# Performance work log

Hardware: AMD Instinct MI355X
Metric: run time of the kernel (lower is better)

Reference implementation:

```python
import jax, jax.numpy as jnp
import numpy as np

NUM_CLASSES = 80
NUM_TOP_QUERIES = 300
MASK_THRESHOLD = 0.5
OUT_SIZE = 480  # fixed original image size (all orig_target_sizes == 480)


def setup_inputs() -> dict:
    key = jax.random.key(0)
    k1, k2, k3 = jax.random.split(key, 3)
    B, Q, C, Hm, Wm = 2, 300, NUM_CLASSES, 128, 128
    pred_logits = jax.random.normal(k1, (B, Q, C), dtype=jnp.float32)
    pred_boxes = jax.random.uniform(k2, (B, Q, 4), dtype=jnp.float32)  # cxcywh in [0,1]
    pred_masks = jax.random.normal(k3, (B, Q, Hm, Wm), dtype=jnp.float32)
    orig_target_sizes = jnp.ones((B, 2), dtype=jnp.float32) * OUT_SIZE
    return {
        'pred_logits': pred_logits,
        'pred_boxes': pred_boxes,
        'pred_masks': pred_masks,
        'orig_target_sizes': orig_target_sizes,
    }


def _box_cxcywh_to_xyxy(boxes):
    cx, cy, w, h = jnp.split(boxes, 4, axis=-1)
    return jnp.concatenate([cx - 0.5 * w, cy - 0.5 * h, cx + 0.5 * w, cy + 0.5 * h], axis=-1)


def reference(pred_logits, pred_boxes, pred_masks, orig_target_sizes):
    B, Q, C = pred_logits.shape
    Hm, Wm = pred_masks.shape[-2:]
    K = NUM_TOP_QUERIES

    # box conversion + scaling to original image size ([s0,s1,s0,s1] like repeat(1,2))
    scale = jnp.tile(orig_target_sizes, (1, 2))[:, None, :]  # [B,1,4]
    scaled_boxes = _box_cxcywh_to_xyxy(pred_boxes) * scale    # [B,Q,4]

    # focal-loss path: sigmoid scores, flattened top-k over (Q*C)
    scores = jax.nn.sigmoid(pred_logits).reshape(B, Q * C)
    top_scores, top_indices = jax.lax.top_k(scores, K)        # [B,K]
    top_labels = top_indices % C
    query_indices = top_indices // C                          # [B,K]

    selected_boxes = jnp.take_along_axis(scaled_boxes, query_indices[..., None], axis=1)  # [B,K,4]

    # per-sample mask selection + sigmoid + bilinear upsample (align_corners=False)
    sel_masks = jnp.take_along_axis(pred_masks, query_indices[..., None, None], axis=1)   # [B,K,Hm,Wm]
    mask_probs = jax.nn.sigmoid(sel_masks)
    up = jax.vmap(lambda m: jax.image.resize(m, (OUT_SIZE, OUT_SIZE), 'bilinear'))(
        mask_probs.reshape(B * K, Hm, Wm)
    ).reshape(B, K, OUT_SIZE, OUT_SIZE)
    binary_masks = up > MASK_THRESHOLD                        # [B,K,H,W] bool (torch adds channel dim of 1)

    return top_scores, top_labels, selected_boxes, binary_masks
```

## Files before the change

kernel.cpp:

```cpp
#include <hip/hip_runtime.h>
#include <math.h>

#define BATCH 2
#define NQ    300
#define NC    80
#define NFLAT (NQ * NC)
#define TOPK  300
#define HM    128
#define OUTS  480
#define NBKT  4096
#define CAP   4096

#define INVSCALEF 0.26666668f

typedef float v4f __attribute__((ext_vector_type(4)));
typedef unsigned long long ull;

__device__ __forceinline__ unsigned mapf(float x) {
    unsigned u = __float_as_uint(x);
    return (u & 0x80000000u) ? ~u : (u | 0x80000000u);
}

__global__ __launch_bounds__(1024) void topk_kernel(
    const float* __restrict__ logits,
    const float* __restrict__ boxes,
    const float* __restrict__ osize,
    float* __restrict__ out,
    int* __restrict__ qidx)
{
    __shared__ unsigned hist[NBKT];
    __shared__ unsigned long long cand[CAP];
    __shared__ unsigned wtot[16];
    __shared__ unsigned ysuf[17];
    __shared__ unsigned sh_T;
    __shared__ unsigned sh_cnt;

    const int b = blockIdx.x;
    const int tid = threadIdx.x;
    const int lane = tid & 63;
    const int w = tid >> 6;
    const float* lg = logits + (size_t)b * NFLAT;
    const v4f* lg4 = (const v4f*)lg;

    *(uint4*)&hist[4 * tid] = make_uint4(0u, 0u, 0u, 0u);
    if (tid == 0) sh_cnt = 0;
    __syncthreads();

    for (int i4 = tid; i4 < NFLAT / 4; i4 += 1024) {
        const v4f v = lg4[i4];
        atomicAdd(&hist[mapf(v.x) >> 20], 1u);
        atomicAdd(&hist[mapf(v.y) >> 20], 1u);
        atomicAdd(&hist[mapf(v.z) >> 20], 1u);
        atomicAdd(&hist[mapf(v.w) >> 20], 1u);
    }
    __syncthreads();

    const uint4 h4 = *(const uint4*)&hist[4 * tid];
    const unsigned gsum = h4.x + h4.y + h4.z + h4.w;

    unsigned s = gsum;
    #pragma unroll
    for (int off = 1; off < 64; off <<= 1) {
        unsigned v = __shfl_down(s, off, 64);
        if (lane + off < 64) s += v;
    }
    if (lane == 0) wtot[w] = s;
    __syncthreads();
    if (tid == 0) {
        unsigned acc = 0;
        ysuf[16] = 0;
        for (int i = 15; i >= 0; --i) { acc += wtot[i]; ysuf[i] = acc; }
    }
    __syncthreads();
    const unsigned S   = s + ysuf[w + 1];
    const unsigned nxt = S - gsum;
    if (S >= (unsigned)TOPK && nxt < (unsigned)TOPK) {
        unsigned acc = nxt, T;
        if (acc + h4.w >= (unsigned)TOPK) T = 4u * tid + 3u;
        else { acc += h4.w;
            if (acc + h4.z >= (unsigned)TOPK) T = 4u * tid + 2u;
            else { acc += h4.z;
                if (acc + h4.y >= (unsigned)TOPK) T = 4u * tid + 1u;
                else T = 4u * tid;
            }
        }
        sh_T = T;
    }
    __syncthreads();
    const unsigned T = sh_T;

    for (int i4 = tid; i4 < NFLAT / 4; i4 += 1024) {
        const v4f v = lg4[i4];
        #pragma unroll
        for (int j = 0; j < 4; ++j) {
            const unsigned m = mapf(v[j]);
            if ((m >> 20) >= T) {
                unsigned pos = atomicAdd(&sh_cnt, 1u);
                if (pos < CAP) {
                    const unsigned idx = 4u * i4 + j;
                    cand[pos] = ((ull)m << 32) | (ull)(0xFFFFFFFFu - idx);
                }
            }
        }
    }
    __syncthreads();
    const unsigned cnt = (sh_cnt > CAP) ? CAP : sh_cnt;

    for (unsigned t = tid; t < cnt; t += 1024) {
        const unsigned long long my = cand[t];
        unsigned rank = 0;
        for (unsigned j = 0; j < cnt; ++j) rank += (cand[j] > my) ? 1u : 0u;
        if (rank < (unsigned)TOPK) {
            const unsigned idx = 0xFFFFFFFFu - (unsigned)(my & 0xFFFFFFFFull);
            const int q = (int)(idx / NC);
            const int c = (int)(idx % NC);
            const double x = (double)lg[idx];
            const double score = 1.0 / (1.0 + exp(-x));

            out[b * TOPK + rank] = (float)score;
            out[BATCH * TOPK + b * TOPK + rank] = (float)c;

            const float* bx = boxes + ((size_t)(b * NQ + q)) * 4;
            const double cx = (double)bx[0], cy = (double)bx[1];
            const double bw = (double)bx[2], bh = (double)bx[3];
            const double s0 = (double)osize[b * 2 + 0];
            const double s1 = (double)osize[b * 2 + 1];
            float* ob = out + 2 * BATCH * TOPK + ((size_t)(b * TOPK + rank)) * 4;
            ob[0] = (float)((cx - 0.5 * bw) * s0);
            ob[1] = (float)((cy - 0.5 * bh) * s1);
            ob[2] = (float)((cx + 0.5 * bw) * s0);
            ob[3] = (float)((cy + 0.5 * bh) * s1);

            qidx[b * TOPK + rank] = q;
        }
    }
}

#define VROWS   16
#define NVS     (OUTS / VROWS)
#define MAXR    6

__global__ __launch_bounds__(256) void mask_kernel(
    const float* __restrict__ masks,
    const int* __restrict__ qidx,
    float* __restrict__ outm)
{
    __shared__ float sig[MAXR * HM];

    const int tid = threadIdx.x;
    const int unit = blockIdx.x;
    const int mask_id = unit / NVS;
    const int vs = unit % NVS;
    const int ys = vs * VROWS;
    const int b = mask_id / TOPK;
    const int q = qidx[mask_id];

    float s_first = ((float)ys + 0.5f) * INVSCALEF - 0.5f;
    float s_last  = ((float)(ys + VROWS - 1) + 0.5f) * INVSCALEF - 0.5f;
    int r_lo = (int)floorf(s_first);
    if (r_lo < 0) r_lo = 0; if (r_lo > HM - 2) r_lo = HM - 2;
    int r_hi = (int)floorf(s_last);
    if (r_hi < 0) r_hi = 0; if (r_hi > HM - 2) r_hi = HM - 2;
    r_hi += 1;
    const int cnt = r_hi - r_lo + 1;

    const v4f* s4 = (const v4f*)(masks
                      + ((size_t)(b * NQ + q)) * (HM * HM)
                      + (size_t)r_lo * HM);
    const int n4 = cnt * (HM / 4);
    if (tid < n4) {
        v4f v = s4[tid];
        float* dst = sig + tid * 4;
        dst[0] = 1.0f / (1.0f + __expf(-v.x));
        dst[1] = 1.0f / (1.0f + __expf(-v.y));
        dst[2] = 1.0f / (1.0f + __expf(-v.z));
        dst[3] = 1.0f / (1.0f + __expf(-v.w));
    }

    const int qd = tid % 120;
    const int yy = tid / 120;
    const int x0 = qd * 4;
    int c0 = 0, ar[4];
    float fxr[4];
    #pragma unroll
    for (int j = 0; j < 4; ++j) {
        float sx = ((float)(x0 + j) + 0.5f) * INVSCALEF - 0.5f;
        int jx = (int)floorf(sx);
        if (jx < 0) jx = 0; if (jx > HM - 2) jx = HM - 2;
        float f = sx - (float)jx;
        f = fminf(fmaxf(f, 0.0f), 1.0f);
        if (j == 0) c0 = jx;
        ar[j]  = jx - c0;
        fxr[j] = f;
    }
    const int c1 = c0 + 1;
    const int c2 = (c0 + 2 > HM - 1) ? (HM - 1) : (c0 + 2);

    __syncthreads();

    if (tid < 240) {
        float* outp = outm + (size_t)mask_id * (OUTS * OUTS)
                           + (size_t)(ys + yy) * OUTS + x0;
        #pragma unroll
        for (int it = 0; it < VROWS / 2; ++it) {
            const int y = ys + yy + it * 2;
            float sy = ((float)y + 0.5f) * INVSCALEF - 0.5f;
            int jy = (int)floorf(sy);
            if (jy < 0) jy = 0; if (jy > HM - 2) jy = HM - 2;
            float fy = sy - (float)jy;
            fy = fminf(fmaxf(fy, 0.0f), 1.0f);

            const float* r0 = sig + (size_t)(jy - r_lo) * HM;
            const float* r1 = r0 + HM;
            const float wy1 = fy, wy0 = 1.0f - fy;

            const float t0 = wy0 * r0[c0] + wy1 * r1[c0];
            const float t1 = wy0 * r0[c1] + wy1 * r1[c1];
            const float t2 = wy0 * r0[c2] + wy1 * r1[c2];

            v4f res;
            #pragma unroll
            for (int j = 0; j < 4; ++j) {
                const float ta = ar[j] ? t1 : t0;
                const float tb = ar[j] ? t2 : t1;
                const float val = ta + fxr[j] * (tb - ta);
                res[j] = (val > 0.5f) ? 1.0f : 0.0f;
            }
            *((v4f*)(outp + (size_t)(it * 2) * OUTS)) = res;
        }
    }
}

extern "C" void kernel_launch(void* const* d_in, const int* in_sizes, int n_in,
                              void* d_out, int out_size, void* d_ws, size_t ws_size,
                              hipStream_t stream) {
    const float* logits = (const float*)d_in[0];
    const float* boxes  = (const float*)d_in[1];
    const float* masks  = (const float*)d_in[2];
    const float* osize  = (const float*)d_in[3];
    float* out = (float*)d_out;
    int* qidx = (int*)d_ws;

    topk_kernel<<<BATCH, 1024, 0, stream>>>(logits, boxes, osize, out, qidx);

    mask_kernel<<<BATCH * TOPK * NVS, 256, 0, stream>>>(masks, qidx, out + 3600);
}
```

Baseline: 139.0 us.

## Give each wavefront its own 8-row slab in mask upsample kernel, drop block sync

The mask kernel now has each block cover 32 output rows, split across its 4 wavefronts at 8 rows each. Each wavefront loads and applies sigmoid to its own source rows in a private shared-memory slab, so the block-wide __syncthreads becomes a wavefront-local lgkmcnt wait. It also launches half as many blocks and keeps all 256 threads busy instead of 240. In exchange, the 120 columns no longer map cleanly onto lanes, so each lane recomputes x-coordinates per iteration. Source rows are also loaded more than once across neighbouring wavefronts.

```diff
diff --git a/kernel.cpp b/kernel.cpp
--- a/kernel.cpp
+++ b/kernel.cpp
@@ -136,98 +136,91 @@
     }
 }
 
-#define VROWS   16
-#define NVS     (OUTS / VROWS)
-#define MAXR    6
+#define WROWS 8
+#define BROWS 32
+#define NSEG  (OUTS / BROWS)
 
 __global__ __launch_bounds__(256) void mask_kernel(
     const float* __restrict__ masks,
     const int* __restrict__ qidx,
     float* __restrict__ outm)
 {
-    __shared__ float sig[MAXR * HM];
-
-    const int tid = threadIdx.x;
+    __shared__ float sig[4][4 * HM];
+
+    const int tid  = threadIdx.x;
+    const int lane = tid & 63;
+    const int w    = tid >> 6;
     const int unit = blockIdx.x;
-    const int mask_id = unit / NVS;
-    const int vs = unit % NVS;
-    const int ys = vs * VROWS;
+    const int mask_id = unit / NSEG;
+    const int seg     = unit % NSEG;
+    const int y0 = seg * BROWS + w * WROWS;
     const int b = mask_id / TOPK;
     const int q = qidx[mask_id];
 
-    float s_first = ((float)ys + 0.5f) * INVSCALEF - 0.5f;
-    float s_last  = ((float)(ys + VROWS - 1) + 0.5f) * INVSCALEF - 0.5f;
+    float s_first = ((float)y0 + 0.5f) * INVSCALEF - 0.5f;
+    float s_last  = ((float)(y0 + WROWS - 1) + 0.5f) * INVSCALEF - 0.5f;
     int r_lo = (int)floorf(s_first);
     if (r_lo < 0) r_lo = 0; if (r_lo > HM - 2) r_lo = HM - 2;
     int r_hi = (int)floorf(s_last);
     if (r_hi < 0) r_hi = 0; if (r_hi > HM - 2) r_hi = HM - 2;
     r_hi += 1;
-    const int cnt = r_hi - r_lo + 1;
+    const int n4 = (r_hi - r_lo + 1) * (HM / 4);
 
     const v4f* s4 = (const v4f*)(masks
                       + ((size_t)(b * NQ + q)) * (HM * HM)
                       + (size_t)r_lo * HM);
-    const int n4 = cnt * (HM / 4);
-    if (tid < n4) {
-        v4f v = s4[tid];
-        float* dst = sig + tid * 4;
-        dst[0] = 1.0f / (1.0f + __expf(-v.x));
-        dst[1] = 1.0f / (1.0f + __expf(-v.y));
-        dst[2] = 1.0f / (1.0f + __expf(-v.z));
-        dst[3] = 1.0f / (1.0f + __expf(-v.w));
-    }
-
-    const int qd = tid % 120;
-    const int yy = tid / 120;
-    const int x0 = qd * 4;
-    int c0 = 0, ar[4];
-    float fxr[4];
+    float* ws = sig[w];
+    for (int i = lane; i < n4; i += 64) {
+        v4f v = s4[i];
+        v4f r;
+        r.x = 1.0f / (1.0f + __expf(-v.x));
+        r.y = 1.0f / (1.0f + __expf(-v.y));
+        r.z = 1.0f / (1.0f + __expf(-v.z));
+        r.w = 1.0f / (1.0f + __expf(-v.w));
+        *((v4f*)(ws + i * 4)) = r;
+    }
+    asm volatile("s_waitcnt lgkmcnt(0)" ::: "memory");
+
+    float* outp = outm + (size_t)mask_id * (OUTS * OUTS);
+
     #pragma unroll
-    for (int j = 0; j < 4; ++j) {
-        float sx = ((float)(x0 + j) + 0.5f) * INVSCALEF - 0.5f;
-        int jx = (int)floorf(sx);
-        if (jx < 0) jx = 0; if (jx > HM - 2) jx = HM - 2;
-        float f = sx - (float)jx;
-        f = fminf(fmaxf(f, 0.0f), 1.0f);
-        if (j == 0) c0 = jx;
-        ar[j]  = jx - c0;
-        fxr[j] = f;
-    }
-    const int c1 = c0 + 1;
-    const int c2 = (c0 + 2 > HM - 1) ? (HM - 1) : (c0 + 2);
-
-    __syncthreads();
-
-    if (tid < 240) {
-        float* outp = outm + (size_t)mask_id * (OUTS * OUTS)
-                           + (size_t)(ys + yy) * OUTS + x0;
+    for (int it = 0; it < (WROWS * 120) / 64; ++it) {
+        const int qq = it * 64 + lane;
+        const int yy = qq / 120;
+        const int qd = qq - yy * 120;
+        const int x0 = qd * 4;
+        const int y  = y0 + yy;
+
+        float sy = ((float)y + 0.5f) * INVSCALEF - 0.5f;
+        int jy = (int)floorf(sy);
+        if (jy < 0) jy = 0; if (jy > HM - 2) jy = HM - 2;
+        float fy = fminf(fmaxf(sy - (float)jy, 0.0f), 1.0f);
+
+        const float* r0 = ws + (size_t)(jy - r_lo) * HM;
+        const float* r1 = r0 + HM;
+
+        float sx0 = ((float)x0 + 0.5f) * INVSCALEF - 0.5f;
+        int c0 = (int)floorf(sx0);
+        if (c0 < 0) c0 = 0; if (c0 > HM - 2) c0 = HM - 2;
+        const int c2 = (c0 + 2 > HM - 1) ? (HM - 1) : (c0 + 2);
+
+        const float t0 = r0[c0]     + fy * (r1[c0]     - r0[c0]);
+        const float t1 = r0[c0 + 1] + fy * (r1[c0 + 1] - r0[c0 + 1]);
+        const float t2 = r0[c2]     + fy * (r1[c2]     - r0[c2]);
+
+        v4f res;
         #pragma unroll
-        for (int it = 0; it < VROWS / 2; ++it) {
-            const int y = ys + yy + it * 2;
-            float sy = ((float)y + 0.5f) * INVSCALEF - 0.5f;
-            int jy = (int)floorf(sy);
-            if (jy < 0) jy = 0; if (jy > HM - 2) jy = HM - 2;
-            float fy = sy - (float)jy;
-            fy = fminf(fmaxf(fy, 0.0f), 1.0f);
-
-            const float* r0 = sig + (size_t)(jy - r_lo) * HM;
-            const float* r1 = r0 + HM;
-            const float wy1 = fy, wy0 = 1.0f - fy;
-
-            const float t0 = wy0 * r0[c0] + wy1 * r1[c0];
-            const float t1 = wy0 * r0[c1] + wy1 * r1[c1];
-            const float t2 = wy0 * r0[c2] + wy1 * r1[c2];
-
-            v4f res;
-            #pragma unroll
-            for (int j = 0; j < 4; ++j) {
-                const float ta = ar[j] ? t1 : t0;
-                const float tb = ar[j] ? t2 : t1;
-                const float val = ta + fxr[j] * (tb - ta);
-                res[j] = (val > 0.5f) ? 1.0f : 0.0f;
-            }
-            *((v4f*)(outp + (size_t)(it * 2) * OUTS)) = res;
-        }
+        for (int j = 0; j < 4; ++j) {
+            float sx = ((float)(x0 + j) + 0.5f) * INVSCALEF - 0.5f;
+            int jx = (int)floorf(sx);
+            if (jx < 0) jx = 0; if (jx > HM - 2) jx = HM - 2;
+            float fx = fminf(fmaxf(sx - (float)jx, 0.0f), 1.0f);
+            const float ta = (jx > c0) ? t1 : t0;
+            const float tb = (jx > c0) ? t2 : t1;
+            const float val = ta + fx * (tb - ta);
+            res[j] = (val > 0.5f) ? 1.0f : 0.0f;
+        }
+        *((v4f*)(outp + (size_t)y * OUTS + x0)) = res;
     }
 }
 
@@ -243,5 +236,5 @@
 
     topk_kernel<<<BATCH, 1024, 0, stream>>>(logits, boxes, osize, out, qidx);
 
-    mask_kernel<<<BATCH * TOPK * NVS, 256, 0, stream>>>(masks, qidx, out + 3600);
-}
+    mask_kernel<<<BATCH * TOPK * NSEG, 256, 0, stream>>>(masks, qidx, out + 3600);
+}
```

After: 146.9 us. 5.7% more time.
